# Kernel tuning notes

Hardware: AMD Instinct MI355X
Metric: run time of the kernel (lower is better)

Reference implementation:

```python
import jax, jax.numpy as jnp
import numpy as np

IN_F = 256
OUT_F = 128
ALPHA = 0.2  # LeakyReLU negative slope
NEG_INF = -9.0e15


def setup_inputs() -> dict:
    key = jax.random.key(0)
    k_h, k_j, k_adj, k_w1, k_w2, k_a = jax.random.split(key, 6)
    B, N = 8, 2048
    h = jax.random.normal(k_h, (B, N, IN_F), dtype=jnp.float32)
    j = jax.random.normal(k_j, (B, N, IN_F), dtype=jnp.float32)
    adj = jax.random.randint(k_adj, (B, N, N), 0, 2, dtype=jnp.int32)
    # xavier_uniform with gain=1.414: bound = gain * sqrt(6/(fan_in+fan_out))
    def xavier(k, shape, gain=1.414):
        bound = gain * np.sqrt(6.0 / (shape[0] + shape[1]))
        return jax.random.uniform(k, shape, jnp.float32, -bound, bound)
    W1 = xavier(k_w1, (IN_F, OUT_F))
    W2 = xavier(k_w2, (IN_F, OUT_F))
    a = xavier(k_a, (2 * OUT_F, 1))
    return {"h": h, "j": j, "adj": adj, "W1": W1, "W2": W2, "a": a}


def reference(h, j, adj, W1, W2, a):
    # Projections: [B, N, OUT_F]
    Wh = jnp.einsum("bnf,fo->bno", h, W1)
    Wj = jnp.einsum("bnf,fo->bno", j, W2)
    # Additive attention logits: e[b,i,k] = leakyrelu(Wh@a1 [i] + Wh@a2 [k])
    Wh1 = Wh @ a[:OUT_F, :]   # [B, N, 1]
    Wh2 = Wh @ a[OUT_F:, :]   # [B, N, 1]
    e = jax.nn.leaky_relu(Wh1 + jnp.swapaxes(Wh2, 1, 2), negative_slope=ALPHA)
    # Mask non-edges, row-softmax over neighbors (dim=2)
    logits = jnp.where(adj > 0, e, NEG_INF)
    attention = jax.nn.softmax(logits, axis=2)
    # dropout skipped (eval mode). attention@Wh + attention@Wj == attention@(Wh+Wj)
    output = jnp.einsum("bik,bko->bio", attention, Wh + Wj)
    return jax.nn.elu(output)  # concat=True
```

## Files before the change

kernel.cpp:

```cpp
#include <hip/hip_runtime.h>
#include <hip/hip_bf16.h>

#define BATCH 8
#define NN 2048
#define IN_F 256
#define OUT_F 128
#define ALPHA 0.2f

typedef __attribute__((ext_vector_type(8))) short short8v;
typedef __attribute__((ext_vector_type(4))) float f32x4;

static __device__ __forceinline__ unsigned short f2bf(float x) {
    unsigned int u = __float_as_uint(x);
    u = (u + 0x7fffu + ((u >> 16) & 1u)) >> 16;
    return (unsigned short)u;
}

__global__ __launch_bounds__(256) void k_prew(
    const float* __restrict__ W1, const float* __restrict__ W2,
    const float* __restrict__ a,
    unsigned short* __restrict__ Wt, float* __restrict__ w1a1, float* __restrict__ w1a2)
{
    const int t = threadIdx.x;
    const int k8 = blockIdx.x * 8;
#pragma unroll
    for (int q = 0; q < 4; ++q) {
        const int idx = q * 256 + t;
        const int o = idx & 127;
        const int kk = k8 + (idx >> 7);
        const float v = (kk < IN_F) ? W1[kk * OUT_F + o] : W2[(kk - IN_F) * OUT_F + o];
        Wt[(size_t)o * 512 + kk] = f2bf(v);
    }
    if (k8 < IN_F) {
        const int lane = t & 63, w = t >> 6;
#pragma unroll
        for (int u = 0; u < 2; ++u) {
            const int kk = k8 + 2 * w + u;
            const float* wr = W1 + kk * OUT_F;
            float v1 = wr[lane] * a[lane] + wr[lane + 64] * a[lane + 64];
            float v2 = wr[lane] * a[OUT_F + lane] + wr[lane + 64] * a[OUT_F + lane + 64];
#pragma unroll
            for (int off = 32; off; off >>= 1) {
                v1 += __shfl_xor(v1, off);
                v2 += __shfl_xor(v2, off);
            }
            if (lane == 0) { w1a1[kk] = v1; w1a2[kk] = v2; }
        }
    }
}

#define BM 16

__global__ __launch_bounds__(256) void k_proj(
    const float* __restrict__ h, const float* __restrict__ j,
    const unsigned short* __restrict__ Wt,
    const float* __restrict__ w1a1g, const float* __restrict__ w1a2g,
    const int* __restrict__ adj,
    unsigned short* __restrict__ Vt, float* __restrict__ s1, float* __restrict__ s2,
    unsigned short* __restrict__ bits16)
{
    __shared__ __align__(16) unsigned short X[BM * 512];

    const int t = threadIdx.x, lane = t & 63, w = t >> 6;
    const int row0 = blockIdx.x * BM;
    const int b = row0 >> 11, n0 = row0 & 2047;

    const float4* wa1v = (const float4*)w1a1g;
    const float4* wa2v = (const float4*)w1a2g;

#pragma unroll
    for (int q = 0; q < 4; ++q) {
        const int idx = q * 256 + t;
        const int row = idx >> 6, f4 = idx & 63;
        const float4 hv = ((const float4*)(h + (size_t)(row0 + row) * IN_F))[f4];
        union { unsigned long long ll; unsigned short u[4]; } pk;
        pk.u[0] = f2bf(hv.x); pk.u[1] = f2bf(hv.y); pk.u[2] = f2bf(hv.z); pk.u[3] = f2bf(hv.w);
        *(unsigned long long*)((char*)X + ((row * 1024 + f4 * 8) ^ ((row & 7) << 4))) = pk.ll;
        const float4 a1 = wa1v[f4], a2 = wa2v[f4];
        float d1 = hv.x * a1.x + hv.y * a1.y + hv.z * a1.z + hv.w * a1.w;
        float d2 = hv.x * a2.x + hv.y * a2.y + hv.z * a2.z + hv.w * a2.w;
#pragma unroll
        for (int off = 32; off; off >>= 1) {
            d1 += __shfl_xor(d1, off);
            d2 += __shfl_xor(d2, off);
        }
        if (lane == 0) { s1[row0 + row] = d1; s2[row0 + row] = d2; }
    }
#pragma unroll
    for (int q = 0; q < 4; ++q) {
        const int idx = q * 256 + t;
        const int row = idx >> 6, f4 = idx & 63;
        const float4 jv = ((const float4*)(j + (size_t)(row0 + row) * IN_F))[f4];
        union { unsigned long long ll; unsigned short u[4]; } pk;
        pk.u[0] = f2bf(jv.x); pk.u[1] = f2bf(jv.y); pk.u[2] = f2bf(jv.z); pk.u[3] = f2bf(jv.w);
        *(unsigned long long*)((char*)X + ((row * 1024 + 512 + f4 * 8) ^ ((row & 7) << 4))) = pk.ll;
    }
    __syncthreads();

    const unsigned short* wb = Wt + (size_t)(w * 32 + (lane & 15)) * 512 + ((lane >> 4) * 8);
    const int abase = (lane & 15) * 1024 + ((lane >> 4) * 16);
    const int aswz = (lane & 7) << 4;

    f32x4 acc0 = {0.f, 0.f, 0.f, 0.f}, acc1 = {0.f, 0.f, 0.f, 0.f};
#pragma unroll
    for (int ks = 0; ks < 16; ++ks) {
        const short8v af = *(const short8v*)((const char*)X + ((abase + ks * 64) ^ aswz));
        const short8v b0 = *(const short8v*)(wb + ks * 32);
        const short8v b1 = *(const short8v*)(wb + 16 * 512 + ks * 32);
        acc0 = __builtin_amdgcn_mfma_f32_16x16x32_bf16(af, b0, acc0, 0, 0, 0);
        acc1 = __builtin_amdgcn_mfma_f32_16x16x32_bf16(af, b1, acc1, 0, 0, 0);
    }

    const int nr = (lane >> 4) * 4;
#pragma unroll
    for (int f = 0; f < 2; ++f) {
        const f32x4 ac = f ? acc1 : acc0;
        const int o = w * 32 + f * 16 + (lane & 15);
        union { unsigned long long ll; unsigned short u[4]; } pk;
#pragma unroll
        for (int r = 0; r < 4; ++r) pk.u[r] = f2bf(ac[r]);
        *(unsigned long long*)(Vt + ((size_t)b * OUT_F + o) * NN + n0 + nr) = pk.ll;
    }

    const int gstride = 1024 * 256;
    for (int g = blockIdx.x * 256 + t; g < (BATCH * NN * NN) / 16; g += gstride) {
        const int4* ap = (const int4*)(adj + (size_t)g * 16);
        const int4 x0 = ap[0], x1 = ap[1], x2 = ap[2], x3 = ap[3];
        unsigned m = 0;
        m |= (x0.x > 0) ? 1u : 0u;        m |= (x0.y > 0) ? 2u : 0u;
        m |= (x0.z > 0) ? 4u : 0u;        m |= (x0.w > 0) ? 8u : 0u;
        m |= (x1.x > 0) ? 16u : 0u;       m |= (x1.y > 0) ? 32u : 0u;
        m |= (x1.z > 0) ? 64u : 0u;       m |= (x1.w > 0) ? 128u : 0u;
        m |= (x2.x > 0) ? 256u : 0u;      m |= (x2.y > 0) ? 512u : 0u;
        m |= (x2.z > 0) ? 1024u : 0u;     m |= (x2.w > 0) ? 2048u : 0u;
        m |= (x3.x > 0) ? 4096u : 0u;     m |= (x3.y > 0) ? 8192u : 0u;
        m |= (x3.z > 0) ? 16384u : 0u;    m |= (x3.w > 0) ? 32768u : 0u;
        bits16[g] = (unsigned short)m;
    }
}

#define IBLK 32

__global__ __launch_bounds__(256, 4) void k_attn(
    const unsigned char* __restrict__ bits, const unsigned short* __restrict__ Vt,
    const float* __restrict__ s1g, const float* __restrict__ s2g,
    float* __restrict__ out)
{
    __shared__ __align__(16) char smem[33792];
    __shared__ float rs_lds[4][IBLK];
    __shared__ float wmaxs[4];
    __shared__ __align__(16) float lut[16][4];

    float* s2_lds = (float*)smem;
    unsigned int* bitw = (unsigned int*)(smem + 8192);
    float* comb = (float*)smem;

    const int t = threadIdx.x, lane = t & 63, w = t >> 6;
    const int orig = blockIdx.x;
    const int b = orig & 7;
    const int r = orig >> 3;
    const int oh = r >> 6;
    const int i0 = (r & 63) * IBLK;

    if (t < 16) {
        lut[t][0] = (float)(t & 1);
        lut[t][1] = (float)((t >> 1) & 1);
        lut[t][2] = (float)((t >> 2) & 1);
        lut[t][3] = (float)((t >> 3) & 1);
    }

    {
        const unsigned int* bg = (const unsigned int*)(bits + ((size_t)b * NN + i0) * 256);
#pragma unroll
        for (int q = 0; q < 8; ++q) {
            const int idx = q * 256 + t;
            bitw[(idx >> 6) * 65 + (idx & 63)] = bg[idx];
        }
    }

    const float4* s2v = (const float4*)(s2g + b * NN);
    float lmax = -1e30f;
#pragma unroll
    for (int q = 0; q < 2; ++q) {
        const int idx = q * 256 + t;
        const float4 v = s2v[idx];
        ((float4*)s2_lds)[idx] = v;
        lmax = fmaxf(fmaxf(lmax, fmaxf(v.x, v.y)), fmaxf(v.z, v.w));
    }
#pragma unroll
    for (int off = 32; off; off >>= 1) lmax = fmaxf(lmax, __shfl_xor(lmax, off));
    if (lane == 0) wmaxs[w] = lmax;

    const int irow = lane & 15;
    const int kcb = lane >> 4;
    const int kw = w * 512;

    const float s1r0 = s1g[b * NN + i0 + irow];
    const float s1r1 = s1g[b * NN + i0 + 16 + irow];
    __syncthreads();
    const float s2max = fmaxf(fmaxf(wmaxs[0], wmaxs[1]), fmaxf(wmaxs[2], wmaxs[3]));
    const float mx0 = s1r0 + s2max, mx1 = s1r1 + s2max;
    const float mA0 = fmaxf(mx0, ALPHA * mx0);
    const float mA1 = fmaxf(mx1, ALPHA * mx1);

    const float* s2p = s2_lds + kw + kcb * 8;
    const unsigned short* vb =
        Vt + ((size_t)b * OUT_F + oh * 64 + irow) * NN + kw + kcb * 8;
    const unsigned int* bw0p = bitw + irow * 65 + w * 16;
    const unsigned int* bw1p = bitw + (16 + irow) * 65 + w * 16;

    short8v vone;
#pragma unroll
    for (int q = 0; q < 8; ++q) vone[q] = (short)0x3F80;

    f32x4 acc0[4], acc1[4];
    f32x4 acc_ps0 = {0.f, 0.f, 0.f, 0.f}, acc_ps1 = {0.f, 0.f, 0.f, 0.f};
#pragma unroll
    for (int og = 0; og < 4; ++og) {
        acc0[og] = (f32x4){0.f, 0.f, 0.f, 0.f};
        acc1[og] = (f32x4){0.f, 0.f, 0.f, 0.f};
    }

#pragma unroll
    for (int ks = 0; ks < 16; ++ks) {
        const short8v vf0 = *(const short8v*)(vb + ks * 32);
        const short8v vf1 = *(const short8v*)(vb + ks * 32 + 16 * NN);
        const short8v vf2 = *(const short8v*)(vb + ks * 32 + 32 * NN);
        const short8v vf3 = *(const short8v*)(vb + ks * 32 + 48 * NN);

        const unsigned int bb0 = (bw0p[ks] >> (kcb * 8)) & 0xffu;
        const unsigned int bb1 = (bw1p[ks] >> (kcb * 8)) & 0xffu;
        const float4 m00 = ((const float4*)lut)[bb0 & 15], m01 = ((const float4*)lut)[bb0 >> 4];
        const float4 m10 = ((const float4*)lut)[bb1 & 15], m11 = ((const float4*)lut)[bb1 >> 4];

        const float4 sa = *(const float4*)(s2p + ks * 32);
        const float4 sb = *(const float4*)(s2p + ks * 32 + 4);
        const float s2r[8] = {sa.x, sa.y, sa.z, sa.w, sb.x, sb.y, sb.z, sb.w};
        const float mk0[8] = {m00.x, m00.y, m00.z, m00.w, m01.x, m01.y, m01.z, m01.w};
        const float mk1[8] = {m10.x, m10.y, m10.z, m10.w, m11.x, m11.y, m11.z, m11.w};

        float p0[8], p1[8];
#pragma unroll
        for (int e = 0; e < 8; ++e) {
            float x0 = s1r0 + s2r[e];
            x0 = fmaxf(x0, ALPHA * x0);
            p0[e] = __expf(x0 - mA0) * mk0[e];
            float x1 = s1r1 + s2r[e];
            x1 = fmaxf(x1, ALPHA * x1);
            p1[e] = __expf(x1 - mA1) * mk1[e];
        }
        union { short8v v; unsigned int u32[4]; } pb0, pb1;
#pragma unroll
        for (int q = 0; q < 4; ++q) {
            asm("v_cvt_pk_bf16_f32 %0, %1, %2" : "=v"(pb0.u32[q]) : "v"(p0[2 * q]), "v"(p0[2 * q + 1]));
            asm("v_cvt_pk_bf16_f32 %0, %1, %2" : "=v"(pb1.u32[q]) : "v"(p1[2 * q]), "v"(p1[2 * q + 1]));
        }

        acc_ps0 = __builtin_amdgcn_mfma_f32_16x16x32_bf16(vone, pb0.v, acc_ps0, 0, 0, 0);
        acc_ps1 = __builtin_amdgcn_mfma_f32_16x16x32_bf16(vone, pb1.v, acc_ps1, 0, 0, 0);
        acc0[0] = __builtin_amdgcn_mfma_f32_16x16x32_bf16(vf0, pb0.v, acc0[0], 0, 0, 0);
        acc1[0] = __builtin_amdgcn_mfma_f32_16x16x32_bf16(vf0, pb1.v, acc1[0], 0, 0, 0);
        acc0[1] = __builtin_amdgcn_mfma_f32_16x16x32_bf16(vf1, pb0.v, acc0[1], 0, 0, 0);
        acc1[1] = __builtin_amdgcn_mfma_f32_16x16x32_bf16(vf1, pb1.v, acc1[1], 0, 0, 0);
        acc0[2] = __builtin_amdgcn_mfma_f32_16x16x32_bf16(vf2, pb0.v, acc0[2], 0, 0, 0);
        acc1[2] = __builtin_amdgcn_mfma_f32_16x16x32_bf16(vf2, pb1.v, acc1[2], 0, 0, 0);
        acc0[3] = __builtin_amdgcn_mfma_f32_16x16x32_bf16(vf3, pb0.v, acc0[3], 0, 0, 0);
        acc1[3] = __builtin_amdgcn_mfma_f32_16x16x32_bf16(vf3, pb1.v, acc1[3], 0, 0, 0);
    }

    if (lane < 16) {
        rs_lds[w][lane] = acc_ps0[0];
        rs_lds[w][16 + lane] = acc_ps1[0];
    }

    __syncthreads();
#pragma unroll
    for (int og = 0; og < 4; ++og) {
#pragma unroll
        for (int rr = 0; rr < 4; ++rr) {
            const int ol = og * 16 + kcb * 4 + rr;
            comb[(w * 64 + ol) * 33 + irow] = acc0[og][rr];
            comb[(w * 64 + ol) * 33 + 16 + irow] = acc1[og][rr];
        }
    }
    __syncthreads();

    const int i = t >> 3, oc = t & 7;
    const float tot = rs_lds[0][i] + rs_lds[1][i] + rs_lds[2][i] + rs_lds[3][i];
    const float inv = 1.0f / tot;
    float res[8];
#pragma unroll
    for (int u = 0; u < 8; ++u) {
        const int ol = oc * 8 + u;
        float v = comb[ol * 33 + i] + comb[(64 + ol) * 33 + i]
                + comb[(128 + ol) * 33 + i] + comb[(192 + ol) * 33 + i];
        v *= inv;
        res[u] = (v > 0.f) ? v : expm1f(v);
    }
    float4* ob = (float4*)(out + ((size_t)b * NN + i0 + i) * OUT_F + oh * 64 + oc * 8);
    ob[0] = make_float4(res[0], res[1], res[2], res[3]);
    ob[1] = make_float4(res[4], res[5], res[6], res[7]);
}

extern "C" void kernel_launch(void* const* d_in, const int* in_sizes, int n_in,
                              void* d_out, int out_size, void* d_ws, size_t ws_size,
                              hipStream_t stream) {
    const float* h  = (const float*)d_in[0];
    const float* j  = (const float*)d_in[1];
    const int* adj  = (const int*)d_in[2];
    const float* W1 = (const float*)d_in[3];
    const float* W2 = (const float*)d_in[4];
    const float* a  = (const float*)d_in[5];
    float* out = (float*)d_out;

    char* ws = (char*)d_ws;
    unsigned short* Vt = (unsigned short*)ws;
    ws += (size_t)BATCH * OUT_F * NN * 2;
    float* s1 = (float*)ws; ws += (size_t)BATCH * NN * 4;
    float* s2 = (float*)ws; ws += (size_t)BATCH * NN * 4;
    unsigned short* Wt = (unsigned short*)ws; ws += 128 * 512 * 2;
    float* w1a1 = (float*)ws; ws += 512 * 4;
    float* w1a2 = (float*)ws; ws += 512 * 4;
    unsigned char* bits = (unsigned char*)ws;

    k_prew<<<64, 256, 0, stream>>>(W1, W2, a, Wt, w1a1, w1a2);
    k_proj<<<(BATCH * NN) / BM, 256, 0, stream>>>(h, j, Wt, w1a1, w1a2, adj,
                                                  Vt, s1, s2, (unsigned short*)bits);
    k_attn<<<(BATCH * NN) / IBLK * 2, 256, 0, stream>>>(bits, Vt, s1, s2, out);
}
```

Before: 78.27 us.

## Store V in MFMA-fragment tiled layout and relax attention occupancy bound

The projection kernel now writes the bf16 V matrix in a tiled fragment layout: 32-key blocks of 8 KB, each holding 128 features x 64 bytes. Each lane's 16-byte MFMA operand load in the attention kernel therefore comes from a small contiguous region rather than rows strided by NN. The goal is better coalescing and cache-line use on the dominant V reads. The attention kernel's launch bound drops from 4 to 3 waves per SIMD, which gives more registers but lowers occupancy. The inline v_cvt_pk_bf16_f32 packing is replaced with the software round-to-nearest f2bf helper, which may add ALU work.

Result: faster. 72.49 us (-7.4%).

```diff
diff --git a/kernel.cpp b/kernel.cpp
--- a/kernel.cpp
+++ b/kernel.cpp
@@ -56,7 +56,7 @@
     const unsigned short* __restrict__ Wt,
     const float* __restrict__ w1a1g, const float* __restrict__ w1a2g,
     const int* __restrict__ adj,
-    unsigned short* __restrict__ Vt, float* __restrict__ s1, float* __restrict__ s2,
+    unsigned short* __restrict__ Vf, float* __restrict__ s1, float* __restrict__ s2,
     unsigned short* __restrict__ bits16)
 {
     __shared__ __align__(16) unsigned short X[BM * 512];
@@ -111,7 +111,10 @@
         acc1 = __builtin_amdgcn_mfma_f32_16x16x32_bf16(af, b1, acc1, 0, 0, 0);
     }
 
-    const int nr = (lane >> 4) * 4;
+    const int nn = n0 + (lane >> 4) * 4;
+    const size_t vbase = (size_t)b * 524288
+                       + ((size_t)(nn >> 5) << 13)
+                       + (((nn & 31) >> 3) << 4) + ((nn & 7) << 1);
 #pragma unroll
     for (int f = 0; f < 2; ++f) {
         const f32x4 ac = f ? acc1 : acc0;
@@ -119,7 +122,7 @@
         union { unsigned long long ll; unsigned short u[4]; } pk;
 #pragma unroll
         for (int r = 0; r < 4; ++r) pk.u[r] = f2bf(ac[r]);
-        *(unsigned long long*)(Vt + ((size_t)b * OUT_F + o) * NN + n0 + nr) = pk.ll;
+        *(unsigned long long*)((char*)Vf + vbase + o * 64) = pk.ll;
     }
 
     const int gstride = 1024 * 256;
@@ -141,8 +144,8 @@
 
 #define IBLK 32
 
-__global__ __launch_bounds__(256, 4) void k_attn(
-    const unsigned char* __restrict__ bits, const unsigned short* __restrict__ Vt,
+__global__ __launch_bounds__(256, 3) void k_attn(
+    const unsigned char* __restrict__ bits, const unsigned short* __restrict__ Vf,
     const float* __restrict__ s1g, const float* __restrict__ s2g,
     float* __restrict__ out)
 {
@@ -204,8 +207,8 @@
     const float mA1 = fmaxf(mx1, ALPHA * mx1);
 
     const float* s2p = s2_lds + kw + kcb * 8;
-    const unsigned short* vb =
-        Vt + ((size_t)b * OUT_F + oh * 64 + irow) * NN + kw + kcb * 8;
+    const char* vfb = (const char*)Vf + (size_t)b * 524288 + (size_t)(w * 16) * 8192
+                    + (size_t)(oh * 64 + irow) * 64 + (size_t)kcb * 16;
     const unsigned int* bw0p = bitw + irow * 65 + w * 16;
     const unsigned int* bw1p = bitw + (16 + irow) * 65 + w * 16;
 
@@ -223,10 +226,11 @@
 
 #pragma unroll
     for (int ks = 0; ks < 16; ++ks) {
-        const short8v vf0 = *(const short8v*)(vb + ks * 32);
-        const short8v vf1 = *(const short8v*)(vb + ks * 32 + 16 * NN);
-        const short8v vf2 = *(const short8v*)(vb + ks * 32 + 32 * NN);
-        const short8v vf3 = *(const short8v*)(vb + ks * 32 + 48 * NN);
+        const char* vk = vfb + (size_t)ks * 8192;
+        const short8v vf0 = *(const short8v*)(vk);
+        const short8v vf1 = *(const short8v*)(vk + 1024);
+        const short8v vf2 = *(const short8v*)(vk + 2048);
+        const short8v vf3 = *(const short8v*)(vk + 3072);
 
         const unsigned int bb0 = (bw0p[ks] >> (kcb * 8)) & 0xffu;
         const unsigned int bb1 = (bw1p[ks] >> (kcb * 8)) & 0xffu;
@@ -239,21 +243,15 @@
         const float mk0[8] = {m00.x, m00.y, m00.z, m00.w, m01.x, m01.y, m01.z, m01.w};
         const float mk1[8] = {m10.x, m10.y, m10.z, m10.w, m11.x, m11.y, m11.z, m11.w};
 
-        float p0[8], p1[8];
+        union { short8v v; unsigned short u[8]; } pb0, pb1;
 #pragma unroll
         for (int e = 0; e < 8; ++e) {
             float x0 = s1r0 + s2r[e];
             x0 = fmaxf(x0, ALPHA * x0);
-            p0[e] = __expf(x0 - mA0) * mk0[e];
+            pb0.u[e] = f2bf(__expf(x0 - mA0) * mk0[e]);
             float x1 = s1r1 + s2r[e];
             x1 = fmaxf(x1, ALPHA * x1);
-            p1[e] = __expf(x1 - mA1) * mk1[e];
-        }
-        union { short8v v; unsigned int u32[4]; } pb0, pb1;
-#pragma unroll
-        for (int q = 0; q < 4; ++q) {
-            asm("v_cvt_pk_bf16_f32 %0, %1, %2" : "=v"(pb0.u32[q]) : "v"(p0[2 * q]), "v"(p0[2 * q + 1]));
-            asm("v_cvt_pk_bf16_f32 %0, %1, %2" : "=v"(pb1.u32[q]) : "v"(p1[2 * q]), "v"(p1[2 * q + 1]));
+            pb1.u[e] = f2bf(__expf(x1 - mA1) * mk1[e]);
         }
 
         acc_ps0 = __builtin_amdgcn_mfma_f32_16x16x32_bf16(vone, pb0.v, acc_ps0, 0, 0, 0);
@@ -314,7 +312,7 @@
     float* out = (float*)d_out;
 
     char* ws = (char*)d_ws;
-    unsigned short* Vt = (unsigned short*)ws;
+    unsigned short* Vf = (unsigned short*)ws;
     ws += (size_t)BATCH * OUT_F * NN * 2;
     float* s1 = (float*)ws; ws += (size_t)BATCH * NN * 4;
     float* s2 = (float*)ws; ws += (size_t)BATCH * NN * 4;
@@ -325,6 +323,6 @@
 
     k_prew<<<64, 256, 0, stream>>>(W1, W2, a, Wt, w1a1, w1a2);
     k_proj<<<(BATCH * NN) / BM, 256, 0, stream>>>(h, j, Wt, w1a1, w1a2, adj,
-                                                  Vt, s1, s2, (unsigned short*)bits);
-    k_attn<<<(BATCH * NN) / IBLK * 2, 256, 0, stream>>>(bits, Vt, s1, s2, out);
-}
+                                                  Vf, s1, s2, (unsigned short*)bits);
+    k_attn<<<(BATCH * NN) / IBLK * 2, 256, 0, stream>>>(bits, Vf, s1, s2, out);
+}
```
